# Kernel tuning notes

Measured on AMD Instinct MI355X. Metric: run time of the kernel, lower is better.

## Reference

```python
import jax, jax.numpy as jnp
import numpy as np

D = 128          # embedding dim
N_INIT = 100000  # number of initial (axiom) clauses
L = 64           # topological levels of derived clauses
M = 4096         # derived clauses per level
N_THAX = 2000    # distinct axiom-name (thax) embeddings
N_SINE = 32      # sine-level embeddings
N_RULES = 256    # distinct inference rules (each with its own 2-ary MLP)
N_TOT = N_INIT + L * M


def setup_inputs() -> dict:
    key = jax.random.key(0)
    ks = jax.random.split(key, 10)
    rng = np.random.default_rng(0)
    # parents of level-l nodes point to any node created strictly earlier
    parents = np.stack(
        [rng.integers(0, N_INIT + l * M, size=(M, 2)) for l in range(L)]
    ).astype(np.int32)  # [L, M, 2]
    return {
        "thax_table": jax.random.normal(ks[0], (N_THAX, D), jnp.float32) * 0.1,
        "sine_table": jax.random.normal(ks[1], (N_SINE, D), jnp.float32) * 0.1,
        "rule_W": jax.random.normal(ks[2], (N_RULES, 2 * D, D), jnp.float32) * (1.0 / np.sqrt(2 * D)),
        "rule_b": jax.random.normal(ks[3], (N_RULES, D), jnp.float32) * 0.01,
        "eval_w": jax.random.normal(ks[4], (D,), jnp.float32) * (1.0 / np.sqrt(D)),
        "eval_b": jax.random.normal(ks[5], (1,), jnp.float32) * 0.01,
        "pos_vals": jax.random.uniform(ks[6], (N_TOT,), jnp.float32, 0.01, 1.0),
        "neg_vals": jax.random.uniform(ks[7], (N_TOT,), jnp.float32, 0.01, 1.0),
        "init_thax": jax.random.randint(ks[8], (N_INIT,), 0, N_THAX, jnp.int32),
        "init_sine": jax.random.randint(ks[9], (N_INIT,), 0, N_SINE, jnp.int32),
        "parents": jnp.asarray(parents),
        "rules": jnp.asarray(rng.integers(0, N_RULES, size=(L, M)).astype(np.int32)),
    }


def reference(thax_table, sine_table, rule_W, rule_b, eval_w, eval_b,
              pos_vals, neg_vals, init_thax, init_sine, parents, rules):
    n_init = init_thax.shape[0]
    n_lvl, m = rules.shape
    d = thax_table.shape[1]

    # init nodes: embed = init_embeds[thax]() + sine_embedder(sine)
    init_emb = thax_table[init_thax] + sine_table[init_sine]  # [N_INIT, D]
    store0 = jnp.concatenate(
        [init_emb, jnp.zeros((n_lvl * m, d), init_emb.dtype)], axis=0)  # [N_TOT, D]

    # deriv nodes, level by level: gather 2 parents, per-rule MLP (cat -> Linear -> ReLU)
    def step(store, xs):
        lvl, par, rul = xs                       # par: [M,2] int, rul: [M] int
        pe = store[par].reshape(m, 2 * d)        # gather parent embeddings
        emb = jax.nn.relu(jnp.einsum('mi,mio->mo', pe, rule_W[rul]) + rule_b[rul])
        store = jax.lax.dynamic_update_slice(store, emb, (n_init + lvl * m, 0))
        return store, None

    store, _ = jax.lax.scan(step, store0, (jnp.arange(n_lvl), parents, rules))

    # eval_net + weighted BCEWithLogits (pos_weight = tot_neg / tot_pos)
    logits = store @ eval_w + eval_b[0]          # [N_TOT]
    tot = pos_vals + neg_vals
    y = pos_vals / tot
    pw = jnp.sum(neg_vals) / jnp.sum(pos_vals)
    per_node = pw * y * jax.nn.softplus(-logits) + (1.0 - y) * jax.nn.softplus(logits)
    loss = jnp.sum(tot * per_node).reshape(1)
    posOK = jnp.sum(jnp.where(logits >= 0.0, pos_vals, 0.0))
    negOK = jnp.sum(jnp.where(logits < 0.0, neg_vals, 0.0))
    return (loss, posOK, negOK)
```

## Files before the change

### kernel.cpp

```cpp
#include <hip/hip_runtime.h>

#define D      128
#define NINIT  100000
#define LVLS   64
#define M      4096
#define NRULES 256
#define NTOT   (NINIT + LVLS * M)
#define NTHR   512
#define TILE   32

typedef __attribute__((ext_vector_type(8))) short short8;
typedef __attribute__((ext_vector_type(4))) float floatx4;

#define ST_OFF 256
#define SI_OFF (ST_OFF + (size_t)NTOT * D * 2)
#define RO_OFF (SI_OFF + (size_t)LVLS * M * 4)
#define FL_OFF (RO_OFF + (size_t)LVLS * (NRULES + 1) * 4)

#define CBAR() asm volatile("" ::: "memory")

__device__ __forceinline__ unsigned short f2bf(float x) {
  unsigned u = __float_as_uint(x);
  u += 0x7fffu + ((u >> 16) & 1u);
  return (unsigned short)(u >> 16);
}

__device__ __forceinline__ float softplusf(float x) {
  return fmaxf(x, 0.f) + log1pf(expf(-fabsf(x)));
}

__device__ __forceinline__ void st_sys(unsigned* p, unsigned v) {
  __hip_atomic_store(p, v, __ATOMIC_RELAXED, __HIP_MEMORY_SCOPE_SYSTEM);
}
__device__ __forceinline__ unsigned ld_sys(const unsigned* p) {
  return __hip_atomic_load(p, __ATOMIC_RELAXED, __HIP_MEMORY_SCOPE_SYSTEM);
}
__device__ __forceinline__ void wait_flag(const unsigned* f) {
  int guard = 1 << 17;
  while (__builtin_expect(ld_sys(f) == 0u, 0) && --guard)
    __builtin_amdgcn_s_sleep(1);
  CBAR();
}

__device__ __forceinline__ void gbar_heavy(unsigned* bcnt, unsigned* bgen) {
  __syncthreads();
  if (threadIdx.x == 0) {
    unsigned g = __hip_atomic_load(bgen, __ATOMIC_RELAXED, __HIP_MEMORY_SCOPE_AGENT);
    unsigned v = __hip_atomic_fetch_add(bcnt, 1u, __ATOMIC_ACQ_REL, __HIP_MEMORY_SCOPE_AGENT);
    if (v == gridDim.x - 1) {
      __hip_atomic_store(bcnt, 0u, __ATOMIC_RELAXED, __HIP_MEMORY_SCOPE_AGENT);
      __hip_atomic_fetch_add(bgen, 1u, __ATOMIC_ACQ_REL, __HIP_MEMORY_SCOPE_AGENT);
    } else {
      while (__hip_atomic_load(bgen, __ATOMIC_RELAXED, __HIP_MEMORY_SCOPE_AGENT) == g)
        __builtin_amdgcn_s_sleep(1);
      __builtin_amdgcn_fence(__ATOMIC_ACQUIRE, "agent");
    }
  }
  __syncthreads();
}

__device__ __forceinline__ void gbar_light(unsigned* bcnt, unsigned* bgen) {
  __syncthreads();
  if (threadIdx.x == 0) {
    unsigned g = ld_sys(bgen);
    unsigned v = __hip_atomic_fetch_add(bcnt, 1u, __ATOMIC_RELAXED,
                                        __HIP_MEMORY_SCOPE_SYSTEM);
    if (v == gridDim.x - 1) {
      st_sys(bcnt, 0u);
      st_sys(bgen, g + 1u);
    } else {
      int guard = 1 << 22;
      while (ld_sys(bgen) == g && --guard) __builtin_amdgcn_s_sleep(2);
    }
  }
  __syncthreads();
}

__device__ __forceinline__ bool adv_cursor(int r, const int* __restrict__ ro,
                                           int& l, int& t0, int& off, int& cnt) {
  t0 += TILE;
  while (t0 >= cnt) {
    if (++l >= LVLS) return false;
    off = ro[l * (NRULES + 1) + r];
    cnt = ro[l * (NRULES + 1) + r + 1] - off;
    t0 = 0;
  }
  return true;
}

__global__ __launch_bounds__(NTHR, 2) void fused_kernel(
    const float* __restrict__ thax_table, const float* __restrict__ sine_table,
    const float* __restrict__ rule_W, const float* __restrict__ rule_b,
    const float* __restrict__ eval_w, const float* __restrict__ eval_b,
    const float* __restrict__ pos, const float* __restrict__ neg,
    const int* __restrict__ init_thax, const int* __restrict__ init_sine,
    const int* __restrict__ parents,
    const int* __restrict__ rules,
    unsigned short* __restrict__ store, int* __restrict__ sorted_idx,
    int* __restrict__ rule_off, unsigned* __restrict__ flags,
    float* __restrict__ sums, unsigned* __restrict__ bvars,
    float* __restrict__ out) {
  __shared__ unsigned short pe[TILE * 264];
  __shared__ unsigned short ot[TILE * 136];
  __shared__ int s_sid[2][TILE];
  __shared__ int s_cnt[NRULES];
  __shared__ int s_base[NRULES + 1];
  __shared__ float racc[3];

  unsigned* bcnt = bvars;
  unsigned* bgen = bvars + 1;

  const int r = blockIdx.x;
  const int tid = threadIdx.x;
  const int wave = tid >> 6, lane = tid & 63;
  const int col = (wave << 4) + (lane & 15);
  const int node = tid >> 4;
  const int segq = tid & 15;
  const int gid = r * NTHR + tid;
  const int gthreads = NRULES * NTHR;

  short8 bf[8];
  {
    const float* Wr = rule_W + (size_t)r * (2 * D * D);
    const int krow_base = (lane >> 4) * 8;
#pragma unroll
    for (int ks = 0; ks < 8; ++ks) {
      union { short8 s; unsigned short us[8]; } c;
#pragma unroll
      for (int j = 0; j < 8; ++j)
        c.us[j] = f2bf(Wr[(size_t)(ks * 32 + krow_base + j) * D + col]);
      bf[ks] = c.s;
    }
  }
  const float bias = rule_b[r * D + col];

  if (r < LVLS) {
    const int l = r;
    const int* rl = rules + (size_t)l * M;
    if (tid < NRULES) s_cnt[tid] = 0;
    __syncthreads();
    for (int m = tid; m < M; m += NTHR) atomicAdd(&s_cnt[rl[m]], 1);
    __syncthreads();
    if (tid == 0) {
      int run = 0;
      for (int q = 0; q < NRULES; ++q) { s_base[q] = run; run += s_cnt[q]; }
      s_base[NRULES] = run;
    }
    __syncthreads();
    if (tid < NRULES) {
      rule_off[(size_t)l * (NRULES + 1) + tid] = s_base[tid];
      s_cnt[tid] = s_base[tid];
    }
    if (tid == 0) rule_off[(size_t)l * (NRULES + 1) + NRULES] = M;
    __syncthreads();
    for (int m = tid; m < M; m += NTHR) {
      int p = atomicAdd(&s_cnt[rl[m]], 1);
      sorted_idx[(size_t)l * M + p] = m;
    }
  }

  for (int idx = gid; idx < NINIT * 16; idx += gthreads) {
    int nd = idx >> 4, sg = idx & 15;
    const float4* t = (const float4*)(thax_table + (size_t)init_thax[nd] * D) + sg * 2;
    const float4* s = (const float4*)(sine_table + (size_t)init_sine[nd] * D) + sg * 2;
    float4 a0 = t[0], a1 = t[1], b0 = s[0], b1 = s[1];
    float v[8] = {a0.x + b0.x, a0.y + b0.y, a0.z + b0.z, a0.w + b0.w,
                  a1.x + b1.x, a1.y + b1.y, a1.z + b1.z, a1.w + b1.w};
    uint4 pk;
    pk.x = (unsigned)f2bf(v[0]) | ((unsigned)f2bf(v[1]) << 16);
    pk.y = (unsigned)f2bf(v[2]) | ((unsigned)f2bf(v[3]) << 16);
    pk.z = (unsigned)f2bf(v[4]) | ((unsigned)f2bf(v[5]) << 16);
    pk.w = (unsigned)f2bf(v[6]) | ((unsigned)f2bf(v[7]) << 16);
    *(uint4*)(store + (size_t)nd * D + sg * 8) = pk;
  }

  {
    float sp = 0.f, sn = 0.f;
    for (int i = gid; i < NTOT; i += gthreads) {
      sp += pos[i];
      sn += neg[i];
    }
    for (int m = 32; m; m >>= 1) {
      sp += __shfl_xor(sp, m, 64);
      sn += __shfl_xor(sn, m, 64);
    }
    if (lane == 0) {
      atomicAdd(&sums[0], sp);
      atomicAdd(&sums[1], sn);
    }
  }

  gbar_heavy(bcnt, bgen);

  int lL = -1, t0L = 0, offL = 0, cntL = 0;

  bool validA = adv_cursor(r, rule_off, lL, t0L, offL, cntL);
  int lA = lL, t0A = t0L, cntA = cntL;
  int parA0 = 0, parA1 = 0;
  bool lateA0 = false, lateA1 = false;
  uint4 gA0 = {0, 0, 0, 0}, gA1 = {0, 0, 0, 0};
  if (validA) {
    int gj = t0A + node; if (gj > cntA - 1) gj = cntA - 1;
    int sid = sorted_idx[(size_t)lA * M + offL + gj];
    parA0 = parents[((size_t)lA * M + sid) * 2 + 0];
    parA1 = parents[((size_t)lA * M + sid) * 2 + 1];
    if (parA0 >= NINIT) wait_flag(flags + (parA0 - NINIT));
    if (parA1 >= NINIT) wait_flag(flags + (parA1 - NINIT));
    gA0 = *(const uint4*)(store + (size_t)parA0 * D + segq * 8);
    gA1 = *(const uint4*)(store + (size_t)parA1 * D + segq * 8);
    if (segq == 0) s_sid[0][node] = sid;
  }

  bool validB = validA && adv_cursor(r, rule_off, lL, t0L, offL, cntL);
  int lB = lL, t0B = t0L, cntB = cntL;
  int sidB = 0, parB0 = 0, parB1 = 0;
  unsigned fB0 = 1u, fB1 = 1u;
  if (validB) {
    int gj = t0B + node; if (gj > cntB - 1) gj = cntB - 1;
    sidB = sorted_idx[(size_t)lB * M + offL + gj];
    parB0 = parents[((size_t)lB * M + sidB) * 2 + 0];
    parB1 = parents[((size_t)lB * M + sidB) * 2 + 1];
    fB0 = parB0 >= NINIT ? ld_sys(flags + (parB0 - NINIT)) : 1u;
    fB1 = parB1 >= NINIT ? ld_sys(flags + (parB1 - NINIT)) : 1u;
  }

  bool validC = validB && adv_cursor(r, rule_off, lL, t0L, offL, cntL);
  int lC = lL, t0C = t0L, cntC = cntL;
  int sidC = 0, parC0 = 0, parC1 = 0;
  if (validC) {
    int gj = t0C + node; if (gj > cntC - 1) gj = cntC - 1;
    sidC = sorted_idx[(size_t)lC * M + offL + gj];
    parC0 = parents[((size_t)lC * M + sidC) * 2 + 0];
    parC1 = parents[((size_t)lC * M + sidC) * 2 + 1];
  }

  bool validD = validC && adv_cursor(r, rule_off, lL, t0L, offL, cntL);
  int lD = lL, t0D = t0L, offD = offL, cntD = cntL;

  int p = 0;
  while (validA) {
    if (lateA0) {
      wait_flag(flags + (parA0 - NINIT));
      gA0 = *(const uint4*)(store + (size_t)parA0 * D + segq * 8);
    }
    if (lateA1) {
      wait_flag(flags + (parA1 - NINIT));
      gA1 = *(const uint4*)(store + (size_t)parA1 * D + segq * 8);
    }

    *(uint4*)(pe + node * 264 + segq * 8) = gA0;
    *(uint4*)(pe + node * 264 + 128 + segq * 8) = gA1;
    __syncthreads();
    if (validB && segq == 0) s_sid[p ^ 1][node] = sidB;

    floatx4 acc0 = {0.f, 0.f, 0.f, 0.f}, acc1 = {0.f, 0.f, 0.f, 0.f};
#pragma unroll
    for (int ks = 0; ks < 8; ++ks) {
      short8 a0 = *(const short8*)(pe + (lane & 15) * 264 + ks * 32 + (lane >> 4) * 8);
      short8 a1 = *(const short8*)(pe + (16 + (lane & 15)) * 264 + ks * 32 + (lane >> 4) * 8);
      acc0 = __builtin_amdgcn_mfma_f32_16x16x32_bf16(a0, bf[ks], acc0, 0, 0, 0);
      acc1 = __builtin_amdgcn_mfma_f32_16x16x32_bf16(a1, bf[ks], acc1, 0, 0, 0);
    }
#pragma unroll
    for (int reg = 0; reg < 4; ++reg) {
      int row = (lane >> 4) * 4 + reg;
      float v0 = acc0[reg] + bias;
      float v1 = acc1[reg] + bias;
      ot[row * 136 + col] = f2bf(v0 > 0.f ? v0 : 0.f);
      ot[(16 + row) * 136 + col] = f2bf(v1 > 0.f ? v1 : 0.f);
    }
    __syncthreads();

    const int n_baseA = NINIT + lA * M;
    int nsid[4]; bool inr[4];
#pragma unroll
    for (int k = 0; k < 4; ++k) {
      int nd = wave + 8 * k;
      nsid[k] = s_sid[p][nd];
      inr[k] = (t0A + nd) < cntA;
      if (inr[k])
        st_sys((unsigned*)(store + (size_t)(n_baseA + nsid[k]) * D) + lane,
               *(const unsigned*)(ot + nd * 136 + lane * 2));
    }
    CBAR();

    bool lateB0 = validB && parB0 >= NINIT && fB0 == 0u;
    bool lateB1 = validB && parB1 >= NINIT && fB1 == 0u;
    uint4 gB0, gB1;
    {
      const unsigned short* a0 =
          (validB && !lateB0) ? store + (size_t)parB0 * D : store;
      const unsigned short* a1 =
          (validB && !lateB1) ? store + (size_t)parB1 * D : store;
      gB0 = *(const uint4*)(a0 + segq * 8);
      gB1 = *(const uint4*)(a1 + segq * 8);
    }
    unsigned fC0 = 1u, fC1 = 1u;
    if (validC) {
      fC0 = ld_sys(flags + (parC0 >= NINIT ? parC0 - NINIT : 0));
      fC1 = ld_sys(flags + (parC1 >= NINIT ? parC1 - NINIT : 0));
      if (parC0 < NINIT) fC0 = 1u;
      if (parC1 < NINIT) fC1 = 1u;
    }
    int sidD = 0, parD0 = 0, parD1 = 0;
    if (validD) {
      int gj = t0D + node; if (gj > cntD - 1) gj = cntD - 1;
      sidD = sorted_idx[(size_t)lD * M + offD + gj];
      parD0 = parents[((size_t)lD * M + sidD) * 2 + 0];
      parD1 = parents[((size_t)lD * M + sidD) * 2 + 1];
    }
    CBAR();

    if (validD) asm volatile("s_waitcnt vmcnt(6)" ::: "memory");
    else        asm volatile("s_waitcnt vmcnt(0)" ::: "memory");

    if (lane == 0) {
#pragma unroll
      for (int k = 0; k < 4; ++k)
        if (inr[k]) st_sys(flags + lA * M + nsid[k], 1u);
    }
    CBAR();

    gA0 = gB0; gA1 = gB1; lateA0 = lateB0; lateA1 = lateB1;
    parA0 = parB0; parA1 = parB1;
    lA = lB; t0A = t0B; cntA = cntB; validA = validB;
    sidB = sidC; parB0 = parC0; parB1 = parC1; fB0 = fC0; fB1 = fC1;
    lB = lC; t0B = t0C; cntB = cntC; validB = validC;
    sidC = sidD; parC0 = parD0; parC1 = parD1;
    lC = lD; t0C = t0D; cntC = cntD; validC = validD;
    validD = validC && adv_cursor(r, rule_off, lL, t0L, offL, cntL);
    lD = lL; t0D = t0L; offD = offL; cntD = cntL;
    p ^= 1;
  }

  gbar_light(bcnt, bgen);

  {
    float a_loss = 0.f, a_pos = 0.f, a_neg = 0.f;
    const float pw = sums[1] / sums[0];
    const float eb = eval_b[0];
    const float4* wv = (const float4*)eval_w;

    for (int nd = gid; nd < NTOT; nd += gthreads) {
      const uint4* v = (const uint4*)(store + (size_t)nd * D);
      float dot = 0.f;
#pragma unroll
      for (int k = 0; k < 16; ++k) {
        uint4 u = v[k];
        float4 w0 = wv[k * 2], w1 = wv[k * 2 + 1];
        dot += __uint_as_float(u.x << 16) * w0.x +
               __uint_as_float(u.x & 0xffff0000u) * w0.y +
               __uint_as_float(u.y << 16) * w0.z +
               __uint_as_float(u.y & 0xffff0000u) * w0.w +
               __uint_as_float(u.z << 16) * w1.x +
               __uint_as_float(u.z & 0xffff0000u) * w1.y +
               __uint_as_float(u.w << 16) * w1.z +
               __uint_as_float(u.w & 0xffff0000u) * w1.w;
      }
      float logit = dot + eb;
      float pp = pos[nd], nn = neg[nd];
      float tot = pp + nn, y = pp / tot;
      a_loss += tot * (pw * y * softplusf(-logit) + (1.f - y) * softplusf(logit));
      if (logit >= 0.f) a_pos += pp; else a_neg += nn;
    }

    for (int m = 32; m; m >>= 1) {
      a_loss += __shfl_xor(a_loss, m, 64);
      a_pos  += __shfl_xor(a_pos,  m, 64);
      a_neg  += __shfl_xor(a_neg,  m, 64);
    }
    if (tid == 0) { racc[0] = 0.f; racc[1] = 0.f; racc[2] = 0.f; }
    __syncthreads();
    if (lane == 0) {
      atomicAdd(&racc[0], a_loss);
      atomicAdd(&racc[1], a_pos);
      atomicAdd(&racc[2], a_neg);
    }
    __syncthreads();
    if (tid == 0) {
      atomicAdd(&out[0], racc[0]);
      atomicAdd(&out[1], racc[1]);
      atomicAdd(&out[2], racc[2]);
    }
  }
}

extern "C" void kernel_launch(void* const* d_in, const int* in_sizes, int n_in,
                              void* d_out, int out_size, void* d_ws, size_t ws_size,
                              hipStream_t stream) {
  const float* thax_table = (const float*)d_in[0];
  const float* sine_table = (const float*)d_in[1];
  const float* rule_W     = (const float*)d_in[2];
  const float* rule_b     = (const float*)d_in[3];
  const float* eval_w     = (const float*)d_in[4];
  const float* eval_b     = (const float*)d_in[5];
  const float* pos_vals   = (const float*)d_in[6];
  const float* neg_vals   = (const float*)d_in[7];
  const int*   init_thax  = (const int*)d_in[8];
  const int*   init_sine  = (const int*)d_in[9];
  const int*   parents    = (const int*)d_in[10];
  const int*   rules      = (const int*)d_in[11];

  float* out = (float*)d_out;
  char* ws = (char*)d_ws;
  float* sums = (float*)ws;
  unsigned* bvars = (unsigned*)(ws + 128);
  unsigned short* store = (unsigned short*)(ws + ST_OFF);
  int* sorted_idx = (int*)(ws + SI_OFF);
  int* rule_off   = (int*)(ws + RO_OFF);
  unsigned* flags = (unsigned*)(ws + FL_OFF);

  (void)hipMemsetAsync(d_out, 0, 3 * sizeof(float), stream);
  (void)hipMemsetAsync(d_ws, 0, 256, stream);
  (void)hipMemsetAsync(ws + FL_OFF, 0, (size_t)LVLS * M * 4, stream);

  void* args[] = {&thax_table, &sine_table, &rule_W, &rule_b, &eval_w, &eval_b,
                  &pos_vals, &neg_vals, &init_thax, &init_sine, &parents,
                  &rules, &store, &sorted_idx, &rule_off, &flags, &sums,
                  &bvars, &out};
  (void)hipLaunchCooperativeKernel((void*)fused_kernel, dim3(NRULES),
                                   dim3(NTHR), args, 0, stream);
}
```

Baseline: 421.9 us.

## Publish per-node ready flags earlier and poll late parent flags jointly

Flags for each finished node are now set right after that node's own store is drained, using graded vmcnt waits, instead of after all prefetch loads complete. Late-parent flags are re-read ahead of time and both parents are polled in one combined loop. The init phase now writes through system-scope stores and uses the light barrier in place of the heavy acquire/release barrier. The aim is to shorten the dependency chain between producing and consuming blocks. The risks are memory-ordering weakness from the relaxed barrier and extra cost from scalarized system-scope stores in init.

```diff
diff --git a/kernel.cpp b/kernel.cpp
--- a/kernel.cpp
+++ b/kernel.cpp
@@ -40,23 +40,6 @@
   while (__builtin_expect(ld_sys(f) == 0u, 0) && --guard)
     __builtin_amdgcn_s_sleep(1);
   CBAR();
-}
-
-__device__ __forceinline__ void gbar_heavy(unsigned* bcnt, unsigned* bgen) {
-  __syncthreads();
-  if (threadIdx.x == 0) {
-    unsigned g = __hip_atomic_load(bgen, __ATOMIC_RELAXED, __HIP_MEMORY_SCOPE_AGENT);
-    unsigned v = __hip_atomic_fetch_add(bcnt, 1u, __ATOMIC_ACQ_REL, __HIP_MEMORY_SCOPE_AGENT);
-    if (v == gridDim.x - 1) {
-      __hip_atomic_store(bcnt, 0u, __ATOMIC_RELAXED, __HIP_MEMORY_SCOPE_AGENT);
-      __hip_atomic_fetch_add(bgen, 1u, __ATOMIC_ACQ_REL, __HIP_MEMORY_SCOPE_AGENT);
-    } else {
-      while (__hip_atomic_load(bgen, __ATOMIC_RELAXED, __HIP_MEMORY_SCOPE_AGENT) == g)
-        __builtin_amdgcn_s_sleep(1);
-      __builtin_amdgcn_fence(__ATOMIC_ACQUIRE, "agent");
-    }
-  }
-  __syncthreads();
 }
 
 __device__ __forceinline__ void gbar_light(unsigned* bcnt, unsigned* bgen) {
@@ -148,14 +131,17 @@
     }
     __syncthreads();
     if (tid < NRULES) {
-      rule_off[(size_t)l * (NRULES + 1) + tid] = s_base[tid];
+      st_sys((unsigned*)&rule_off[(size_t)l * (NRULES + 1) + tid],
+             (unsigned)s_base[tid]);
       s_cnt[tid] = s_base[tid];
     }
-    if (tid == 0) rule_off[(size_t)l * (NRULES + 1) + NRULES] = M;
+    if (tid == 0)
+      st_sys((unsigned*)&rule_off[(size_t)l * (NRULES + 1) + NRULES],
+             (unsigned)M);
     __syncthreads();
     for (int m = tid; m < M; m += NTHR) {
       int p = atomicAdd(&s_cnt[rl[m]], 1);
-      sorted_idx[(size_t)l * M + p] = m;
+      st_sys((unsigned*)&sorted_idx[(size_t)l * M + p], (unsigned)m);
     }
   }
 
@@ -166,12 +152,11 @@
     float4 a0 = t[0], a1 = t[1], b0 = s[0], b1 = s[1];
     float v[8] = {a0.x + b0.x, a0.y + b0.y, a0.z + b0.z, a0.w + b0.w,
                   a1.x + b1.x, a1.y + b1.y, a1.z + b1.z, a1.w + b1.w};
-    uint4 pk;
-    pk.x = (unsigned)f2bf(v[0]) | ((unsigned)f2bf(v[1]) << 16);
-    pk.y = (unsigned)f2bf(v[2]) | ((unsigned)f2bf(v[3]) << 16);
-    pk.z = (unsigned)f2bf(v[4]) | ((unsigned)f2bf(v[5]) << 16);
-    pk.w = (unsigned)f2bf(v[6]) | ((unsigned)f2bf(v[7]) << 16);
-    *(uint4*)(store + (size_t)nd * D + sg * 8) = pk;
+    unsigned* dst = (unsigned*)(store + (size_t)nd * D + sg * 8);
+    st_sys(dst + 0, (unsigned)f2bf(v[0]) | ((unsigned)f2bf(v[1]) << 16));
+    st_sys(dst + 1, (unsigned)f2bf(v[2]) | ((unsigned)f2bf(v[3]) << 16));
+    st_sys(dst + 2, (unsigned)f2bf(v[4]) | ((unsigned)f2bf(v[5]) << 16));
+    st_sys(dst + 3, (unsigned)f2bf(v[6]) | ((unsigned)f2bf(v[7]) << 16));
   }
 
   {
@@ -190,7 +175,7 @@
     }
   }
 
-  gbar_heavy(bcnt, bgen);
+  gbar_light(bcnt, bgen);
 
   int lL = -1, t0L = 0, offL = 0, cntL = 0;
 
@@ -198,6 +183,7 @@
   int lA = lL, t0A = t0L, cntA = cntL;
   int parA0 = 0, parA1 = 0;
   bool lateA0 = false, lateA1 = false;
+  unsigned reA0 = 1u, reA1 = 1u;
   uint4 gA0 = {0, 0, 0, 0}, gA1 = {0, 0, 0, 0};
   if (validA) {
     int gj = t0A + node; if (gj > cntA - 1) gj = cntA - 1;
@@ -239,13 +225,21 @@
 
   int p = 0;
   while (validA) {
-    if (lateA0) {
-      wait_flag(flags + (parA0 - NINIT));
-      gA0 = *(const uint4*)(store + (size_t)parA0 * D + segq * 8);
-    }
-    if (lateA1) {
-      wait_flag(flags + (parA1 - NINIT));
-      gA1 = *(const uint4*)(store + (size_t)parA1 * D + segq * 8);
+    if (lateA0 || lateA1) {
+      bool n0 = lateA0 && (reA0 == 0u);
+      bool n1 = lateA1 && (reA1 == 0u);
+      if (n0 || n1) {
+        int guard = 1 << 17;
+        while (guard--) {
+          unsigned f0 = n0 ? ld_sys(flags + (parA0 - NINIT)) : 1u;
+          unsigned f1 = n1 ? ld_sys(flags + (parA1 - NINIT)) : 1u;
+          if (f0 != 0u && f1 != 0u) break;
+          __builtin_amdgcn_s_sleep(1);
+        }
+      }
+      CBAR();
+      if (lateA0) gA0 = *(const uint4*)(store + (size_t)parA0 * D + segq * 8);
+      if (lateA1) gA1 = *(const uint4*)(store + (size_t)parA1 * D + segq * 8);
     }
 
     *(uint4*)(pe + node * 264 + segq * 8) = gA0;
@@ -271,18 +265,33 @@
     }
     __syncthreads();
 
-    const int n_baseA = NINIT + lA * M;
-    int nsid[4]; bool inr[4];
-#pragma unroll
-    for (int k = 0; k < 4; ++k) {
-      int nd = wave + 8 * k;
-      nsid[k] = s_sid[p][nd];
-      inr[k] = (t0A + nd) < cntA;
-      if (inr[k])
-        st_sys((unsigned*)(store + (size_t)(n_baseA + nsid[k]) * D) + lane,
-               *(const unsigned*)(ot + nd * 136 + lane * 2));
-    }
-    CBAR();
+    {
+      const int n_baseA = NINIT + lA * M;
+      int nsid[4]; bool inr[4]; int S = 0;
+#pragma unroll
+      for (int k = 0; k < 4; ++k) {
+        int nd = wave + 8 * k;
+        nsid[k] = s_sid[p][nd];
+        inr[k] = (t0A + nd) < cntA;
+        if (inr[k]) {
+          st_sys((unsigned*)(store + (size_t)(n_baseA + nsid[k]) * D) + lane,
+                 *(const unsigned*)(ot + nd * 136 + lane * 2));
+          ++S;
+        }
+      }
+      CBAR();
+#pragma unroll
+      for (int k = 0; k < 4; ++k) {
+        if (inr[k]) {
+          if (S == 4)      asm volatile("s_waitcnt vmcnt(3)" ::: "memory");
+          else if (S == 3) asm volatile("s_waitcnt vmcnt(2)" ::: "memory");
+          else if (S == 2) asm volatile("s_waitcnt vmcnt(1)" ::: "memory");
+          else             asm volatile("s_waitcnt vmcnt(0)" ::: "memory");
+          if (lane == 0) st_sys(flags + lA * M + nsid[k], 1u);
+        }
+      }
+      CBAR();
+    }
 
     bool lateB0 = validB && parB0 >= NINIT && fB0 == 0u;
     bool lateB1 = validB && parB1 >= NINIT && fB1 == 0u;
@@ -295,6 +304,13 @@
       gB0 = *(const uint4*)(a0 + segq * 8);
       gB1 = *(const uint4*)(a1 + segq * 8);
     }
+    int sidD = 0, parD0 = 0, parD1 = 0;
+    if (validD) {
+      int gj = t0D + node; if (gj > cntD - 1) gj = cntD - 1;
+      sidD = sorted_idx[(size_t)lD * M + offD + gj];
+      parD0 = parents[((size_t)lD * M + sidD) * 2 + 0];
+      parD1 = parents[((size_t)lD * M + sidD) * 2 + 1];
+    }
     unsigned fC0 = 1u, fC1 = 1u;
     if (validC) {
       fC0 = ld_sys(flags + (parC0 >= NINIT ? parC0 - NINIT : 0));
@@ -302,26 +318,13 @@
       if (parC0 < NINIT) fC0 = 1u;
       if (parC1 < NINIT) fC1 = 1u;
     }
-    int sidD = 0, parD0 = 0, parD1 = 0;
-    if (validD) {
-      int gj = t0D + node; if (gj > cntD - 1) gj = cntD - 1;
-      sidD = sorted_idx[(size_t)lD * M + offD + gj];
-      parD0 = parents[((size_t)lD * M + sidD) * 2 + 0];
-      parD1 = parents[((size_t)lD * M + sidD) * 2 + 1];
-    }
+    unsigned reB0 = 1u, reB1 = 1u;
+    if (lateB0) reB0 = ld_sys(flags + (parB0 - NINIT));
+    if (lateB1) reB1 = ld_sys(flags + (parB1 - NINIT));
     CBAR();
 
-    if (validD) asm volatile("s_waitcnt vmcnt(6)" ::: "memory");
-    else        asm volatile("s_waitcnt vmcnt(0)" ::: "memory");
-
-    if (lane == 0) {
-#pragma unroll
-      for (int k = 0; k < 4; ++k)
-        if (inr[k]) st_sys(flags + lA * M + nsid[k], 1u);
-    }
-    CBAR();
-
     gA0 = gB0; gA1 = gB1; lateA0 = lateB0; lateA1 = lateB1;
+    reA0 = reB0; reA1 = reB1;
     parA0 = parB0; parA1 = parB1;
     lA = lB; t0A = t0B; cntA = cntB; validA = validB;
     sidB = sidC; parB0 = parC0; parB1 = parC1; fB0 = fC0; fB1 = fC1;
```

After: 425.7 us. Within noise of the previous version (+0.9%).
